# Performance work log

Measured on AMD Instinct MI355X. Metric: run time of the kernel, lower is better.

## Reference

```python
import jax, jax.numpy as jnp
import numpy as np

N_NODES = 100000
N_EDGES = 1600000
HEADS = 2
D_HEAD = 64


def _transformer_conv(x, src, dst, Wq, bq, Wk, bk, Wv, bv, Ws, bs):
    # PyG TransformerConv (concat=True, beta=False, root_weight=True)
    N = x.shape[0]
    H, D = HEADS, D_HEAD
    q = (x @ Wq + bq).reshape(N, H, D)
    k = (x @ Wk + bk).reshape(N, H, D)
    v = (x @ Wv + bv).reshape(N, H, D)
    scale = np.float32(1.0 / np.sqrt(D))
    # per-edge attention logits [E, H]; messages flow src -> dst
    logits = (q[dst] * k[src]).sum(-1) * scale
    m = jax.ops.segment_max(logits, dst, num_segments=N)  # [N, H]
    e = jnp.exp(logits - m[dst])                          # [E, H]
    denom = jax.ops.segment_sum(e, dst, num_segments=N)   # [N, H]
    num = jax.ops.segment_sum(e[:, :, None] * v[src], dst, num_segments=N)  # [N, H, D]
    out = num / jnp.maximum(denom, 1e-16)[:, :, None]
    return out.reshape(N, H * D) + (x @ Ws + bs)


def setup_inputs() -> dict:
    key = jax.random.key(0)
    ks = jax.random.split(key, 16)
    d = {}
    d['x'] = jax.random.normal(ks[0], (N_NODES, 128), dtype=jnp.float32)
    d['edge_index'] = jax.random.randint(ks[1], (2, N_EDGES), 0, N_NODES, dtype=jnp.int64)
    s = 0.05
    d['Wq1'] = jax.random.normal(ks[2], (128, 128), jnp.float32) * s
    d['bq1'] = jnp.zeros((128,), jnp.float32)
    d['Wk1'] = jax.random.normal(ks[3], (128, 128), jnp.float32) * s
    d['bk1'] = jnp.zeros((128,), jnp.float32)
    d['Wv1'] = jax.random.normal(ks[4], (128, 128), jnp.float32) * s
    d['bv1'] = jnp.zeros((128,), jnp.float32)
    d['Ws1'] = jax.random.normal(ks[5], (128, 128), jnp.float32) * s
    d['bs1'] = jnp.zeros((128,), jnp.float32)
    d['Wq2'] = jax.random.normal(ks[6], (128, 128), jnp.float32) * s
    d['bq2'] = jnp.zeros((128,), jnp.float32)
    d['Wk2'] = jax.random.normal(ks[7], (128, 128), jnp.float32) * s
    d['bk2'] = jnp.zeros((128,), jnp.float32)
    d['Wv2'] = jax.random.normal(ks[8], (128, 128), jnp.float32) * s
    d['bv2'] = jnp.zeros((128,), jnp.float32)
    d['Ws2'] = jax.random.normal(ks[9], (128, 128), jnp.float32) * s
    d['bs2'] = jnp.zeros((128,), jnp.float32)
    d['Wc'] = jax.random.normal(ks[10], (128, 40), jnp.float32) * s
    d['bc'] = jnp.zeros((40,), jnp.float32)
    return d


def reference(x, edge_index, Wq1, bq1, Wk1, bk1, Wv1, bv1, Ws1, bs1,
              Wq2, bq2, Wk2, bk2, Wv2, bv2, Ws2, bs2, Wc, bc):
    src, dst = edge_index[0], edge_index[1]
    h = _transformer_conv(x, src, dst, Wq1, bq1, Wk1, bk1, Wv1, bv1, Ws1, bs1)
    h = jax.nn.elu(h)  # dropout is eval-mode no-op
    h = _transformer_conv(h, src, dst, Wq2, bq2, Wk2, bk2, Wv2, bv2, Ws2, bs2)
    return h @ Wc + bc
```

## Files before the change

kernel.cpp:

```cpp
#include <hip/hip_runtime.h>
#include <hip/hip_bf16.h>
#include <math.h>

#define FDIM 128

typedef unsigned int uint;
typedef unsigned short ushort;
typedef __attribute__((ext_vector_type(8))) short short8;
typedef __attribute__((ext_vector_type(4))) float f32x4;
typedef __attribute__((ext_vector_type(2))) uint uintv2;
typedef __attribute__((ext_vector_type(4))) uint uintv4;
typedef __attribute__((ext_vector_type(4))) float floatv4;

__device__ inline ushort f2bf(float f) {
  uint u = __float_as_uint(f);
  uint r = (u + 0x7fffu + ((u >> 16) & 1u)) >> 16;
  return (ushort)r;
}
#define BFLO(u) __uint_as_float(((uint)(u)) << 16)
#define BFHI(u) __uint_as_float((u) & 0xffff0000u)

__device__ inline float dot2bf(uint a, uint b, float c) {
  float d;
  asm("v_dot2_f32_bf16 %0, %1, %2, %3" : "=v"(d) : "v"(a), "v"(b), "v"(c));
  return d;
}


__global__ __launch_bounds__(256) void k_scatter8(const int* __restrict__ ei, int E,
                                                  int N, int* __restrict__ cnt,
                                                  int* __restrict__ ssrc) {
  int part = blockIdx.x & 7;
  int chunk = blockIdx.x >> 3;
  int lo = (int)(((long long)part * N) >> 3);
  int hi = (int)(((long long)(part + 1) * N) >> 3);
  const int* dsts = ei + E;
  int base = chunk * 4096 + threadIdx.x;
#pragma unroll
  for (int i = 0; i < 16; ++i) {
    int e = base + i * 256;
    if (e < E) {
      int d = dsts[e];
      if (d >= lo && d < hi) {
        int pos = atomicAdd(&cnt[d], 1);
        ssrc[((size_t)d << 6) + pos] = ei[e] << 9;
      }
    }
  }
}


__global__ __launch_bounds__(256) void k_cvtw(
    const float* __restrict__ Wq1, const float* __restrict__ Wk1,
    const float* __restrict__ Wv1, const float* __restrict__ Ws1,
    const float* __restrict__ Wq2, const float* __restrict__ Wk2,
    const float* __restrict__ Wv2, const float* __restrict__ Ws2,
    const float* __restrict__ Wc,
    ushort* __restrict__ Wt1, ushort* __restrict__ Wt2,
    ushort* __restrict__ Wct) {
  int idx = blockIdx.x * 256 + threadIdx.x;
  if (idx < 131072) {
    int which = idx >> 16;
    int m = (idx >> 14) & 3;
    int e = idx & 16383;
    int n = e >> 7, k = e & 127;
    const float* W;
    if (which == 0) W = (m == 0) ? Wq1 : (m == 1) ? Wk1 : (m == 2) ? Wv1 : Ws1;
    else            W = (m == 0) ? Wq2 : (m == 1) ? Wk2 : (m == 2) ? Wv2 : Ws2;
    ushort* o = which ? Wt2 : Wt1;
    o[(size_t)(m * 128 + n) * 128 + k] = f2bf(W[k * 128 + n]);
  } else {
    int j = idx - 131072;
    if (j < 48 * 128) {
      int n = j >> 7, k = j & 127;
      float w = (n < 40) ? Wc[k * 40 + n] : 0.f;
      ushort hi = f2bf(w);
      float res = w - BFLO(hi);
      Wct[j] = hi;
      Wct[48 * 128 + j] = f2bf(res);
    }
  }
}


#define LPAD 136

__global__ __launch_bounds__(256) void k_gemm_qkvs(
    const void* __restrict__ Araw, int aF32, const ushort* __restrict__ Wt,
    const float* __restrict__ bq, const float* __restrict__ bk,
    const float* __restrict__ bv, const float* __restrict__ bs,
    ushort* __restrict__ qb, ushort* __restrict__ kvb, ushort* __restrict__ skb,
    int N) {
  __shared__ ushort sA[128 * LPAD];
  __shared__ ushort sB[128 * LPAD];
  int tid = threadIdx.x;
  int bm = blockIdx.x * 128;

  for (int c = tid; c < 128 * 16; c += 256) {
    int r = c >> 4, kc = (c & 15) * 8;
    int gr = bm + r;
    uint4 val = {0, 0, 0, 0};
    if (gr < N) {
      if (aF32) {
        const float* xr = (const float*)Araw + (size_t)gr * 128 + kc;
        floatv4 f0 = *(const floatv4*)xr;
        floatv4 f1 = *(const floatv4*)(xr + 4);
        val.x = (uint)f2bf(f0.x) | ((uint)f2bf(f0.y) << 16);
        val.y = (uint)f2bf(f0.z) | ((uint)f2bf(f0.w) << 16);
        val.z = (uint)f2bf(f1.x) | ((uint)f2bf(f1.y) << 16);
        val.w = (uint)f2bf(f1.z) | ((uint)f2bf(f1.w) << 16);
      } else {
        val = *(const uint4*)((const ushort*)Araw + (size_t)gr * 128 + kc);
      }
    }
    *(uint4*)&sA[r * LPAD + kc] = val;
  }

  int lane = tid & 63, wv = tid >> 6;
  int ml = lane & 15, quad = lane >> 4;
  const ushort* pA0 = &sA[(32 * wv + ml) * LPAD + quad * 8];
  const ushort* pA1 = &sA[(32 * wv + 16 + ml) * LPAD + quad * 8];
  const ushort* pB = &sB[ml * LPAD + quad * 8];

#pragma unroll
  for (int mat = 0; mat < 4; ++mat) {
    __syncthreads();
    for (int c = tid; c < 128 * 16; c += 256) {
      int r = c >> 4, kc = (c & 15) * 8;
      uint4 val = *(const uint4*)&Wt[(size_t)(mat * 128 + r) * 128 + kc];
      *(uint4*)&sB[r * LPAD + kc] = val;
    }
    __syncthreads();

    f32x4 acc0[8] = {}, acc1[8] = {};
#pragma unroll
    for (int k0 = 0; k0 < 128; k0 += 32) {
      short8 a0 = *(const short8*)&pA0[k0];
      short8 a1 = *(const short8*)&pA1[k0];
#pragma unroll
      for (int ct = 0; ct < 8; ++ct) {
        short8 b = *(const short8*)&pB[ct * 16 * LPAD + k0];
        acc0[ct] = __builtin_amdgcn_mfma_f32_16x16x32_bf16(a0, b, acc0[ct], 0, 0, 0);
        acc1[ct] = __builtin_amdgcn_mfma_f32_16x16x32_bf16(a1, b, acc1[ct], 0, 0, 0);
      }
    }
    __syncthreads();

    const float* B = (mat == 0) ? bq : (mat == 1) ? bk : (mat == 2) ? bv : bs;
    float oscale = (mat == 0) ? 0.1803368801f : 1.0f;
    int r0 = 32 * wv + quad * 4;
#pragma unroll
    for (int ct = 0; ct < 8; ++ct) {
      int c = ct * 16 + ml;
      float bias = B[c];
#pragma unroll
      for (int r = 0; r < 4; ++r) {
        sB[(r0 + r) * LPAD + c] = f2bf((acc0[ct][r] + bias) * oscale);
        sB[(r0 + 16 + r) * LPAD + c] = f2bf((acc1[ct][r] + bias) * oscale);
      }
    }
    __syncthreads();

    ushort* obase = (mat == 0) ? qb : (mat == 3) ? skb : kvb;
    int ostride = (mat == 1 || mat == 2) ? 256 : 128;
    int ooff = (mat == 2) ? 128 : 0;
    for (int c = tid; c < 128 * 16; c += 256) {
      int r = c >> 4, kc = (c & 15) * 8;
      int gr = bm + r;
      if (gr < N) {
        uintv4 val = *(const uintv4*)&sB[r * LPAD + kc];
        __builtin_nontemporal_store(
            val, (uintv4*)&obase[(size_t)gr * ostride + ooff + kc]);
      }
    }
  }
}


__global__ __launch_bounds__(256) void k_attn(const ushort* __restrict__ qb,
                                              const ushort* __restrict__ kvb,
                                              const ushort* __restrict__ skb,
                                              const int* __restrict__ cntv,
                                              const int* __restrict__ ssrc,
                                              ushort* __restrict__ outb,
                                              int N, int applyElu) {
  int n = (int)(blockIdx.x * (blockDim.x >> 6)) + (threadIdx.x >> 6);
  int lane = threadIdx.x & 63;
  if (n >= N) return;
  int g = lane >> 4;
  int hl = lane & 15;
  int dim0 = hl * 8;
  int hB = hl << 4;
  const char* kvB = (const char*)kvb;
  uintv4 qu = __builtin_nontemporal_load((const uintv4*)&qb[(size_t)n * FDIM + dim0]);
  int cnt = cntv[n];
  float lsum = 0.f;
  float a0 = 0.f, a1 = 0.f, a2 = 0.f, a3 = 0.f;
  float a4 = 0.f, a5 = 0.f, a6 = 0.f, a7 = 0.f;

#define QKDOT(ku_) dot2bf(ku_.w, qu.w, dot2bf(ku_.z, qu.z,                     \
                    dot2bf(ku_.y, qu.y, dot2bf(ku_.x, qu.x, 0.f))))
#define ACCV(pe_, vu_)                                                         \
  lsum += pe_;                                                                 \
  a0 += pe_ * BFLO(vu_.x); a1 += pe_ * BFHI(vu_.x);                            \
  a2 += pe_ * BFLO(vu_.y); a3 += pe_ * BFHI(vu_.y);                            \
  a4 += pe_ * BFLO(vu_.z); a5 += pe_ * BFHI(vu_.z);                            \
  a6 += pe_ * BFLO(vu_.w); a7 += pe_ * BFHI(vu_.w);

#define EDGE1(T)                                                               \
  {                                                                            \
    int t_ = (T);                                                              \
    int s_ = __shfl(slane, t_, 64);                                            \
    const ushort* p_ = (const ushort*)(kvB + (uint)s_ + hB);                   \
    uintv4 ku_ = *(const uintv4*)p_;                                           \
    uintv4 vu_ = *(const uintv4*)(p_ + 128);                                   \
    float d_ = QKDOT(ku_);                                                     \
    d_ += __shfl_xor(d_, 1, 64);                                               \
    d_ += __shfl_xor(d_, 2, 64);                                               \
    d_ += __shfl_xor(d_, 4, 64);                                               \
    float p_e = (t_ < cnt) ? __builtin_exp2f(d_) : 0.f;                        \
    ACCV(p_e, vu_);                                                            \
  }

  {
    const int* sp = ssrc + ((size_t)n << 6);
    int slane = (lane < cnt) ? __builtin_nontemporal_load(&sp[lane]) : 0;
    int nIter = (cnt + 3) >> 2;
    int it = 0;
    for (; it + 3 <= nIter; it += 3) {
      int t0 = g + 4 * it;
      int s0 = __shfl(slane, t0, 64);
      int s1 = __shfl(slane, t0 + 4, 64);
      int s2 = __shfl(slane, t0 + 8, 64);
      const ushort* p0 = (const ushort*)(kvB + (uint)s0 + hB);
      const ushort* p1 = (const ushort*)(kvB + (uint)s1 + hB);
      const ushort* p2 = (const ushort*)(kvB + (uint)s2 + hB);
      uintv4 k0 = *(const uintv4*)p0, v0 = *(const uintv4*)(p0 + 128);
      uintv4 k1 = *(const uintv4*)p1, v1 = *(const uintv4*)(p1 + 128);
      uintv4 k2 = *(const uintv4*)p2, v2 = *(const uintv4*)(p2 + 128);
      float d0 = QKDOT(k0), d1 = QKDOT(k1), d2 = QKDOT(k2);
      d0 += __shfl_xor(d0, 1, 64); d1 += __shfl_xor(d1, 1, 64);
      d2 += __shfl_xor(d2, 1, 64);
      d0 += __shfl_xor(d0, 2, 64); d1 += __shfl_xor(d1, 2, 64);
      d2 += __shfl_xor(d2, 2, 64);
      d0 += __shfl_xor(d0, 4, 64); d1 += __shfl_xor(d1, 4, 64);
      d2 += __shfl_xor(d2, 4, 64);
      float e0 = (t0     < cnt) ? __builtin_exp2f(d0) : 0.f;
      float e1 = (t0 + 4 < cnt) ? __builtin_exp2f(d1) : 0.f;
      float e2 = (t0 + 8 < cnt) ? __builtin_exp2f(d2) : 0.f;
      ACCV(e0, v0); ACCV(e1, v1); ACCV(e2, v2);
    }
    for (; it < nIter; ++it) {
      EDGE1(g + 4 * it);
    }
  }
#undef EDGE1
#undef ACCV
#undef QKDOT

  lsum += __shfl_xor(lsum, 16, 64);
  a0 += __shfl_xor(a0, 16, 64); a1 += __shfl_xor(a1, 16, 64);
  a2 += __shfl_xor(a2, 16, 64); a3 += __shfl_xor(a3, 16, 64);
  a4 += __shfl_xor(a4, 16, 64); a5 += __shfl_xor(a5, 16, 64);
  a6 += __shfl_xor(a6, 16, 64); a7 += __shfl_xor(a7, 16, 64);
  lsum += __shfl_xor(lsum, 32, 64);
  a0 += __shfl_xor(a0, 32, 64); a1 += __shfl_xor(a1, 32, 64);
  a2 += __shfl_xor(a2, 32, 64); a3 += __shfl_xor(a3, 32, 64);
  a4 += __shfl_xor(a4, 32, 64); a5 += __shfl_xor(a5, 32, 64);
  a6 += __shfl_xor(a6, 32, 64); a7 += __shfl_xor(a7, 32, 64);
  float inv = 1.f / fmaxf(lsum, 1e-16f);
  if (g == 0) {
    uintv4 su = __builtin_nontemporal_load((const uintv4*)&skb[(size_t)n * FDIM + dim0]);
    float r0 = a0 * inv + BFLO(su.x);
    float r1 = a1 * inv + BFHI(su.x);
    float r2 = a2 * inv + BFLO(su.y);
    float r3 = a3 * inv + BFHI(su.y);
    float r4 = a4 * inv + BFLO(su.z);
    float r5 = a5 * inv + BFHI(su.z);
    float r6 = a6 * inv + BFLO(su.w);
    float r7 = a7 * inv + BFHI(su.w);
    if (applyElu) {
      r0 = (r0 > 0.f) ? r0 : (__expf(r0) - 1.f);
      r1 = (r1 > 0.f) ? r1 : (__expf(r1) - 1.f);
      r2 = (r2 > 0.f) ? r2 : (__expf(r2) - 1.f);
      r3 = (r3 > 0.f) ? r3 : (__expf(r3) - 1.f);
      r4 = (r4 > 0.f) ? r4 : (__expf(r4) - 1.f);
      r5 = (r5 > 0.f) ? r5 : (__expf(r5) - 1.f);
      r6 = (r6 > 0.f) ? r6 : (__expf(r6) - 1.f);
      r7 = (r7 > 0.f) ? r7 : (__expf(r7) - 1.f);
    }
    uintv4 p;
    p.x = (uint)f2bf(r0) | ((uint)f2bf(r1) << 16);
    p.y = (uint)f2bf(r2) | ((uint)f2bf(r3) << 16);
    p.z = (uint)f2bf(r4) | ((uint)f2bf(r5) << 16);
    p.w = (uint)f2bf(r6) | ((uint)f2bf(r7) << 16);
    __builtin_nontemporal_store(p, (uintv4*)&outb[(size_t)n * FDIM + dim0]);
  }
}


__global__ __launch_bounds__(256) void k_final(const ushort* __restrict__ H,
                                               const ushort* __restrict__ Wct,
                                               const float* __restrict__ bc,
                                               float* __restrict__ out, int N) {
  __shared__ ushort sH[128 * LPAD];
  __shared__ ushort sW[96 * LPAD];
  int tid = threadIdx.x;
  int bm = blockIdx.x * 128;

  for (int c = tid; c < 128 * 16; c += 256) {
    int r = c >> 4, kc = (c & 15) * 8;
    int gr = bm + r;
    uint4 val = {0, 0, 0, 0};
    if (gr < N) val = *(const uint4*)&H[(size_t)gr * 128 + kc];
    *(uint4*)&sH[r * LPAD + kc] = val;
  }
  for (int c = tid; c < 96 * 16; c += 256) {
    int r = c >> 4, kc = (c & 15) * 8;
    uint4 val = *(const uint4*)&Wct[(size_t)r * 128 + kc];
    *(uint4*)&sW[r * LPAD + kc] = val;
  }
  __syncthreads();

  int lane = tid & 63, wv = tid >> 6;
  int ml = lane & 15, quad = lane >> 4;
  const ushort* pA0 = &sH[(32 * wv + ml) * LPAD + quad * 8];
  const ushort* pA1 = &sH[(32 * wv + 16 + ml) * LPAD + quad * 8];
  const ushort* pBh = &sW[ml * LPAD + quad * 8];
  const ushort* pBl = &sW[(48 + ml) * LPAD + quad * 8];
  f32x4 acc0[3] = {}, acc1[3] = {};
#pragma unroll
  for (int k0 = 0; k0 < 128; k0 += 32) {
    short8 a0 = *(const short8*)&pA0[k0];
    short8 a1 = *(const short8*)&pA1[k0];
#pragma unroll
    for (int ct = 0; ct < 3; ++ct) {
      short8 bh = *(const short8*)&pBh[ct * 16 * LPAD + k0];
      short8 bl = *(const short8*)&pBl[ct * 16 * LPAD + k0];
      acc0[ct] = __builtin_amdgcn_mfma_f32_16x16x32_bf16(a0, bh, acc0[ct], 0, 0, 0);
      acc0[ct] = __builtin_amdgcn_mfma_f32_16x16x32_bf16(a0, bl, acc0[ct], 0, 0, 0);
      acc1[ct] = __builtin_amdgcn_mfma_f32_16x16x32_bf16(a1, bh, acc1[ct], 0, 0, 0);
      acc1[ct] = __builtin_amdgcn_mfma_f32_16x16x32_bf16(a1, bl, acc1[ct], 0, 0, 0);
    }
  }
  __syncthreads();

  float* sO = (float*)sH;
  int r0 = 32 * wv + quad * 4;
#pragma unroll
  for (int ct = 0; ct < 3; ++ct) {
    int c = ct * 16 + ml;
    float bias = (c < 40) ? bc[c] : 0.f;
#pragma unroll
    for (int r = 0; r < 4; ++r) {
      sO[(r0 + r) * 48 + c] = acc0[ct][r] + bias;
      sO[(r0 + 16 + r) * 48 + c] = acc1[ct][r] + bias;
    }
  }
  __syncthreads();

  for (int i = tid; i < 128 * 10; i += 256) {
    int r = i / 10, seg = i % 10;
    int gr = bm + r;
    if (gr < N) {
      floatv4 v = *(const floatv4*)&sO[r * 48 + seg * 4];
      __builtin_nontemporal_store(v, (floatv4*)&out[(size_t)gr * 40 + seg * 4]);
    }
  }
}


#define ALIGN_UP(p) ((char*)(((size_t)(p) + 255) & ~(size_t)255))

extern "C" void kernel_launch(void* const* d_in, const int* in_sizes, int n_in,
                              void* d_out, int out_size, void* d_ws, size_t ws_size,
                              hipStream_t stream) {
  const float* x  = (const float*)d_in[0];
  const int*   ei = (const int*)d_in[1];
  const float* Wq1 = (const float*)d_in[2],  *bq1 = (const float*)d_in[3];
  const float* Wk1 = (const float*)d_in[4],  *bk1 = (const float*)d_in[5];
  const float* Wv1 = (const float*)d_in[6],  *bv1 = (const float*)d_in[7];
  const float* Ws1 = (const float*)d_in[8],  *bs1 = (const float*)d_in[9];
  const float* Wq2 = (const float*)d_in[10], *bq2 = (const float*)d_in[11];
  const float* Wk2 = (const float*)d_in[12], *bk2 = (const float*)d_in[13];
  const float* Wv2 = (const float*)d_in[14], *bv2 = (const float*)d_in[15];
  const float* Ws2 = (const float*)d_in[16], *bs2 = (const float*)d_in[17];
  const float* Wc  = (const float*)d_in[18], *bc  = (const float*)d_in[19];

  int N = in_sizes[0] / FDIM;
  int E = in_sizes[1] / 2;

  char* w = (char*)d_ws;
  ushort* qb  = (ushort*)w; w = ALIGN_UP(w + (size_t)N * 128 * sizeof(ushort));
  ushort* kvb = (ushort*)w; w = ALIGN_UP(w + (size_t)N * 256 * sizeof(ushort));
  ushort* skb = (ushort*)w; w = ALIGN_UP(w + (size_t)N * 128 * sizeof(ushort));
  ushort* ab16 = (ushort*)w; w = ALIGN_UP(w + (size_t)N * 128 * sizeof(ushort));
  ushort* Wt1 = (ushort*)w; w = ALIGN_UP(w + (size_t)512 * 128 * sizeof(ushort));
  ushort* Wt2 = (ushort*)w; w = ALIGN_UP(w + (size_t)512 * 128 * sizeof(ushort));
  ushort* Wct = (ushort*)w; w = ALIGN_UP(w + (size_t)2 * 48 * 128 * sizeof(ushort));
  int* cnt  = (int*)w;      w = ALIGN_UP(w + (size_t)N * sizeof(int));
  int* ssrc = (int*)w;

  int C8 = 8 * ((E + 4095) / 4096);

  hipMemsetAsync(cnt, 0, (size_t)N * sizeof(int), stream);
  k_scatter8<<<C8, 256, 0, stream>>>(ei, E, N, cnt, ssrc);

  k_cvtw<<<536, 256, 0, stream>>>(Wq1, Wk1, Wv1, Ws1, Wq2, Wk2, Wv2, Ws2, Wc,
                                  Wt1, Wt2, Wct);

  int gblocks = (N + 127) / 128;
  int ablocks = (N + 3) / 4;

  k_gemm_qkvs<<<gblocks, 256, 0, stream>>>(x, 1, Wt1, bq1, bk1, bv1, bs1, qb, kvb, skb, N);
  k_attn<<<ablocks, 256, 0, stream>>>(qb, kvb, skb, cnt, ssrc, ab16, N, 1);

  k_gemm_qkvs<<<gblocks, 256, 0, stream>>>(ab16, 0, Wt2, bq2, bk2, bv2, bs2, qb, kvb, skb, N);
  k_attn<<<ablocks, 256, 0, stream>>>(qb, kvb, skb, cnt, ssrc, ab16, N, 0);

  k_final<<<gblocks, 256, 0, stream>>>(ab16, Wct, bc, (float*)d_out, N);
}
```

Baseline: 533.3 us.

## Fuse edge scatter into first QKVS GEMM launch and fold count reset

```diff
diff --git a/kernel.cpp b/kernel.cpp
--- a/kernel.cpp
+++ b/kernel.cpp
@@ -27,11 +27,11 @@
 }
 
 
-__global__ __launch_bounds__(256) void k_scatter8(const int* __restrict__ ei, int E,
-                                                  int N, int* __restrict__ cnt,
-                                                  int* __restrict__ ssrc) {
-  int part = blockIdx.x & 7;
-  int chunk = blockIdx.x >> 3;
+__device__ __forceinline__ void scatter_body(int blk, const int* __restrict__ ei,
+                                             int E, int N, int* __restrict__ cnt,
+                                             int* __restrict__ ssrc) {
+  int part = blk & 7;
+  int chunk = blk >> 3;
   int lo = (int)(((long long)part * N) >> 3);
   int hi = (int)(((long long)(part + 1) * N) >> 3);
   const int* dsts = ei + E;
@@ -57,8 +57,9 @@
     const float* __restrict__ Wv2, const float* __restrict__ Ws2,
     const float* __restrict__ Wc,
     ushort* __restrict__ Wt1, ushort* __restrict__ Wt2,
-    ushort* __restrict__ Wct) {
+    ushort* __restrict__ Wct, int* __restrict__ cnt, int N) {
   int idx = blockIdx.x * 256 + threadIdx.x;
+  if (idx < N) cnt[idx] = 0;
   if (idx < 131072) {
     int which = idx >> 16;
     int m = (idx >> 14) & 3;
@@ -85,8 +86,9 @@
 
 #define LPAD 136
 
-__global__ __launch_bounds__(256) void k_gemm_qkvs(
-    const void* __restrict__ Araw, int aF32, const ushort* __restrict__ Wt,
+__device__ __forceinline__ void gemm_body(
+    int bm, const void* __restrict__ Araw, int aF32,
+    const ushort* __restrict__ Wt,
     const float* __restrict__ bq, const float* __restrict__ bk,
     const float* __restrict__ bv, const float* __restrict__ bs,
     ushort* __restrict__ qb, ushort* __restrict__ kvb, ushort* __restrict__ skb,
@@ -94,7 +96,6 @@
   __shared__ ushort sA[128 * LPAD];
   __shared__ ushort sB[128 * LPAD];
   int tid = threadIdx.x;
-  int bm = blockIdx.x * 128;
 
   for (int c = tid; c < 128 * 16; c += 256) {
     int r = c >> 4, kc = (c & 15) * 8;
@@ -173,6 +174,30 @@
             val, (uintv4*)&obase[(size_t)gr * ostride + ooff + kc]);
       }
     }
+  }
+}
+
+__global__ __launch_bounds__(256) void k_gemm_qkvs(
+    const void* __restrict__ Araw, int aF32, const ushort* __restrict__ Wt,
+    const float* __restrict__ bq, const float* __restrict__ bk,
+    const float* __restrict__ bv, const float* __restrict__ bs,
+    ushort* __restrict__ qb, ushort* __restrict__ kvb, ushort* __restrict__ skb,
+    int N) {
+  gemm_body(blockIdx.x * 128, Araw, aF32, Wt, bq, bk, bv, bs, qb, kvb, skb, N);
+}
+
+__global__ __launch_bounds__(256) void k_gemm1_scatter(
+    const int* __restrict__ ei, int E, int C8,
+    const void* __restrict__ Araw, const ushort* __restrict__ Wt,
+    const float* __restrict__ bq, const float* __restrict__ bk,
+    const float* __restrict__ bv, const float* __restrict__ bs,
+    ushort* __restrict__ qb, ushort* __restrict__ kvb, ushort* __restrict__ skb,
+    int* __restrict__ cnt, int* __restrict__ ssrc, int N) {
+  if ((int)blockIdx.x < C8) {
+    scatter_body(blockIdx.x, ei, E, N, cnt, ssrc);
+  } else {
+    gemm_body(((int)blockIdx.x - C8) * 128, Araw, 1, Wt, bq, bk, bv, bs,
+              qb, kvb, skb, N);
   }
 }
 
@@ -402,20 +427,19 @@
   int* ssrc = (int*)w;
 
   int C8 = 8 * ((E + 4095) / 4096);
-
-  hipMemsetAsync(cnt, 0, (size_t)N * sizeof(int), stream);
-  k_scatter8<<<C8, 256, 0, stream>>>(ei, E, N, cnt, ssrc);
-
-  k_cvtw<<<536, 256, 0, stream>>>(Wq1, Wk1, Wv1, Ws1, Wq2, Wk2, Wv2, Ws2, Wc,
-                                  Wt1, Wt2, Wct);
-
   int gblocks = (N + 127) / 128;
   int ablocks = (N + 3) / 4;
 
-  k_gemm_qkvs<<<gblocks, 256, 0, stream>>>(x, 1, Wt1, bq1, bk1, bv1, bs1, qb, kvb, skb, N);
+  k_cvtw<<<536, 256, 0, stream>>>(Wq1, Wk1, Wv1, Ws1, Wq2, Wk2, Wv2, Ws2, Wc,
+                                  Wt1, Wt2, Wct, cnt, N);
+
+  k_gemm1_scatter<<<C8 + gblocks, 256, 0, stream>>>(
+      ei, E, C8, x, Wt1, bq1, bk1, bv1, bs1, qb, kvb, skb, cnt, ssrc, N);
+
   k_attn<<<ablocks, 256, 0, stream>>>(qb, kvb, skb, cnt, ssrc, ab16, N, 1);
 
   k_gemm_qkvs<<<gblocks, 256, 0, stream>>>(ab16, 0, Wt2, bq2, bk2, bv2, bs2, qb, kvb, skb, N);
+
   k_attn<<<ablocks, 256, 0, stream>>>(qb, kvb, skb, cnt, ssrc, ab16, N, 0);
 
   k_final<<<gblocks, 256, 0, stream>>>(ab16, Wct, bc, (float*)d_out, N);
```

After: 549.4 us. +3.0%, slower.
